# Performance work log

Measured on AMD Instinct MI355X. Metric: run time of the kernel, lower is better.

The kernel has to match this reference:

```python
import jax, jax.numpy as jnp
import numpy as np


def _butter_bandpass_ba(N, w1, w2):
    """Digital Butterworth bandpass design (scipy.signal.iirfilter equivalent),
    fs = 2 half-cycles/sample, output='ba'. Done in float64 numpy at setup time."""
    # analog lowpass prototype (buttap): no zeros, N poles on unit circle, k=1
    p = -np.exp(1j * np.pi * np.arange(-N + 1, N, 2) / (2.0 * N))
    k = 1.0
    fs = 2.0
    warped = 2.0 * fs * np.tan(np.pi * np.array([w1, w2]) / fs)
    bw = warped[1] - warped[0]
    wo = np.sqrt(warped[0] * warped[1])
    # lp2bp_zpk
    p_lp = p * bw / 2.0
    sq = np.sqrt(p_lp ** 2 - wo ** 2)
    p_bp = np.concatenate([p_lp + sq, p_lp - sq])          # 2N poles
    z_bp = np.zeros(N, dtype=complex)                       # N zeros at origin
    k_bp = k * bw ** N
    # bilinear_zpk with fs=2
    fs2 = 2.0 * fs
    z_d = (fs2 + z_bp) / (fs2 - z_bp)
    p_d = (fs2 + p_bp) / (fs2 - p_bp)
    z_d = np.concatenate([z_d, -np.ones(len(p_bp) - len(z_bp))])
    k_d = k_bp * np.real(np.prod(fs2 - z_bp) / np.prod(fs2 - p_bp))
    b = np.real(k_d * np.poly(z_d))
    a = np.real(np.poly(p_d))
    return b, a


def setup_inputs() -> dict:
    key = jax.random.key(0)
    B, T = 512, 65536
    x = jax.random.normal(key, (B, T), dtype=jnp.float32)
    b_np, a_np = _butter_bandpass_ba(4, 0.1, 0.4)           # len 9 each
    return {
        "x": x,
        "b": jnp.asarray(b_np, dtype=jnp.float32),
        "a": jnp.asarray(a_np, dtype=jnp.float32),
    }


def _lfilter(x, b, a):
    """Direct-form II transposed IIR filter with zero initial state.
    x: (B, T); b, a: (M,). Equivalent to torchaudio lfilter (clamp=False)."""
    b = b / a[0]
    a = a / a[0]
    b0 = b[0]
    bt = b[1:]          # (M-1,)
    at = a[1:]          # (M-1,)

    def step(z, xt):
        # z: (B, M-1) delay state, xt: (B,)
        y = b0 * xt + z[:, 0]
        z_new = xt[:, None] * bt[None, :] - y[:, None] * at[None, :]
        z_new = z_new.at[:, :-1].add(z[:, 1:])
        return z_new, y

    z0 = jnp.zeros((x.shape[0], b.shape[0] - 1), dtype=x.dtype)
    _, y = jax.lax.scan(step, z0, x.T)                      # y: (T, B)
    return y.T


def reference(x, b, a):
    # filtfilt: forward pass, then filter the time-reversed result and reverse back
    y = _lfilter(x, b, a)
    y = _lfilter(y[:, ::-1], b, a)[:, ::-1]
    return y
```

## Files before the change

kernel.cpp:

```cpp
#include <hip/hip_runtime.h>

constexpr int CHUNK   = 32;
constexpr int WARM    = 96;
constexpr int BLOCK   = 256;
constexpr int TILE    = BLOCK * CHUNK;
constexpr int WARM_Q  = WARM / 4;
constexpr int TILE_Q  = TILE / 4;
constexpr int STAGE_Q = TILE_Q + WARM_Q;
constexpr int QPT     = CHUNK / 4;

__device__ __forceinline__ int sw(int g) { return g ^ ((g >> 3) & 7); }

template <int DIR>
__global__ __launch_bounds__(BLOCK, 4) void iir_pass(
    const float* __restrict__ x, float* __restrict__ y,
    const float* __restrict__ bc, const float* __restrict__ ac,
    int T, int tilesPerRow)
{
    __shared__ float4 lds[STAGE_Q];

    const int tid     = threadIdx.x;
    const int row     = blockIdx.x / tilesPerRow;
    const int tileIdx = blockIdx.x - row * tilesPerRow;
    const int tileStart = tileIdx * TILE;

    const float* __restrict__ xr = x + (size_t)row * T;
    float* __restrict__       yr = y + (size_t)row * T;

    auto ld4 = [&](int s) -> float4 {
        if (s < 0) return float4{0.f, 0.f, 0.f, 0.f};
        if (DIR == 0) return *(const float4*)(xr + s);
        float4 v = *(const float4*)(xr + (T - 4 - s));
        return float4{v.w, v.z, v.y, v.x};
    };

#pragma unroll
    for (int k = 0; k < (STAGE_Q + BLOCK - 1) / BLOCK; ++k) {
        const int g = k * BLOCK + tid;
        if (g < STAGE_Q) lds[sw(g)] = ld4(tileStart - WARM + 4 * g);
    }

    const float inv = 1.0f / ac[0];
    const float b0  = bc[0] * inv;
    float bt[8], nat[8];
#pragma unroll
    for (int i = 0; i < 8; ++i) {
        bt[i]  = bc[i + 1] * inv;
        nat[i] = -(ac[i + 1] * inv);
    }

    float z[8];
#pragma unroll
    for (int i = 0; i < 8; ++i) z[i] = 0.0f;

    auto step = [&](float xv) -> float {
        const float yv = fmaf(b0, xv, z[0]);
#pragma unroll
        for (int i = 0; i < 7; ++i)
            z[i] = fmaf(nat[i], yv, fmaf(bt[i], xv, z[i + 1]));
        z[7] = fmaf(nat[7], yv, bt[7] * xv);
        return yv;
    };

    __syncthreads();

    const int gw = tid * QPT;
#pragma unroll
    for (int i = 0; i < WARM_Q; ++i) {
        const float4 q = lds[sw(gw + i)];
        step(q.x); step(q.y); step(q.z); step(q.w);
    }

    float4 out[QPT];
#pragma unroll
    for (int j = 0; j < QPT; ++j) {
        const float4 q = lds[sw(gw + WARM_Q + j)];
        float4 o;
        o.x = step(q.x); o.y = step(q.y); o.z = step(q.z); o.w = step(q.w);
        out[j] = o;
    }

    __syncthreads();

#pragma unroll
    for (int j = 0; j < QPT; ++j) lds[sw(gw + j)] = out[j];

    __syncthreads();

#pragma unroll
    for (int k = 0; k < TILE_Q / BLOCK; ++k) {
        const int q = k * BLOCK + tid;
        const float4 v = lds[sw(q)];
        const int s = tileStart + 4 * q;
        if (DIR == 0) {
            *(float4*)(yr + s) = v;
        } else {
            *(float4*)(yr + (T - 4 - s)) = float4{v.w, v.z, v.y, v.x};
        }
    }
}

extern "C" void kernel_launch(void* const* d_in, const int* in_sizes, int n_in,
                              void* d_out, int out_size, void* d_ws, size_t ws_size,
                              hipStream_t stream)
{
    const float* x = (const float*)d_in[0];
    const float* b = (const float*)d_in[1];
    const float* a = (const float*)d_in[2];
    float* out = (float*)d_out;
    float* tmp = (float*)d_ws;

    const int T = 65536;
    const int B = in_sizes[0] / T;
    const int tilesPerRow = T / TILE;
    const int totalBlocks = B * tilesPerRow;

    dim3 block(BLOCK);
    dim3 grid(totalBlocks);

    iir_pass<0><<<grid, block, 0, stream>>>(x,   tmp, b, a, T, tilesPerRow);
    iir_pass<1><<<grid, block, 0, stream>>>(tmp, out, b, a, T, tilesPerRow);
}
```

Before: 307.7 us.

## Process two chunks per thread with packed float2 FMAs and in-place LDS output

Each thread now filters two independent chunks at once using two-wide vector FMAs, aimed at the packed FP32 FMA instruction, with the block size halved so each block still covers the same tile. Output is written back in place into the LDS staging buffer rather than held in registers and rewritten after a barrier, and the store loop reads at the warm-up offset. This is meant to double instruction throughput for the serial recurrence. In exchange it doubles per-thread register state and halves the thread count per block. The extra barrier after warm-up relies on each thread's in-place writes not overlapping any other thread's reads.

```diff
diff --git a/kernel.cpp b/kernel.cpp
--- a/kernel.cpp
+++ b/kernel.cpp
@@ -2,17 +2,32 @@
 
 constexpr int CHUNK   = 32;
 constexpr int WARM    = 96;
-constexpr int BLOCK   = 256;
-constexpr int TILE    = BLOCK * CHUNK;
+constexpr int BLOCK   = 128;
+constexpr int NCHUNK  = 2 * BLOCK;
+constexpr int TILE    = NCHUNK * CHUNK;
 constexpr int WARM_Q  = WARM / 4;
 constexpr int TILE_Q  = TILE / 4;
 constexpr int STAGE_Q = TILE_Q + WARM_Q;
 constexpr int QPT     = CHUNK / 4;
 
+typedef float v2 __attribute__((ext_vector_type(2)));
+
 __device__ __forceinline__ int sw(int g) { return g ^ ((g >> 3) & 7); }
 
+__device__ __forceinline__ v2 fma2(v2 a, v2 b, v2 c) {
+#if defined(__has_builtin)
+#if __has_builtin(__builtin_elementwise_fma)
+    return __builtin_elementwise_fma(a, b, c);
+#else
+    return v2{fmaf(a.x, b.x, c.x), fmaf(a.y, b.y, c.y)};
+#endif
+#else
+    return v2{fmaf(a.x, b.x, c.x), fmaf(a.y, b.y, c.y)};
+#endif
+}
+
 template <int DIR>
-__global__ __launch_bounds__(BLOCK, 4) void iir_pass(
+__global__ __launch_bounds__(BLOCK, 2) void iir_pass(
     const float* __restrict__ x, float* __restrict__ y,
     const float* __restrict__ bc, const float* __restrict__ ac,
     int T, int tilesPerRow)
@@ -41,56 +56,64 @@
     }
 
     const float inv = 1.0f / ac[0];
-    const float b0  = bc[0] * inv;
-    float bt[8], nat[8];
+    const v2 b02 = {bc[0] * inv, bc[0] * inv};
+    v2 bt2[8], nat2[8];
 #pragma unroll
     for (int i = 0; i < 8; ++i) {
-        bt[i]  = bc[i + 1] * inv;
-        nat[i] = -(ac[i + 1] * inv);
+        const float bi = bc[i + 1] * inv;
+        const float ai = -(ac[i + 1] * inv);
+        bt2[i]  = v2{bi, bi};
+        nat2[i] = v2{ai, ai};
     }
 
-    float z[8];
+    v2 z2[8];
 #pragma unroll
-    for (int i = 0; i < 8; ++i) z[i] = 0.0f;
+    for (int i = 0; i < 8; ++i) z2[i] = v2{0.f, 0.f};
 
-    auto step = [&](float xv) -> float {
-        const float yv = fmaf(b0, xv, z[0]);
+    auto step2 = [&](v2 xv) -> v2 {
+        const v2 yv = fma2(b02, xv, z2[0]);
 #pragma unroll
         for (int i = 0; i < 7; ++i)
-            z[i] = fmaf(nat[i], yv, fmaf(bt[i], xv, z[i + 1]));
-        z[7] = fmaf(nat[7], yv, bt[7] * xv);
+            z2[i] = fma2(nat2[i], yv, fma2(bt2[i], xv, z2[i + 1]));
+        z2[7] = fma2(nat2[7], yv, bt2[7] * xv);
         return yv;
     };
 
     __syncthreads();
 
-    const int gw = tid * QPT;
+    const int gA = 8 * tid;
+    const int gB = 8 * tid + (TILE_Q / 2);
+
 #pragma unroll
     for (int i = 0; i < WARM_Q; ++i) {
-        const float4 q = lds[sw(gw + i)];
-        step(q.x); step(q.y); step(q.z); step(q.w);
-    }
-
-    float4 out[QPT];
-#pragma unroll
-    for (int j = 0; j < QPT; ++j) {
-        const float4 q = lds[sw(gw + WARM_Q + j)];
-        float4 o;
-        o.x = step(q.x); o.y = step(q.y); o.z = step(q.z); o.w = step(q.w);
-        out[j] = o;
+        const float4 qA = lds[sw(gA + i)];
+        const float4 qB = lds[sw(gB + i)];
+        step2(v2{qA.x, qB.x}); step2(v2{qA.y, qB.y});
+        step2(v2{qA.z, qB.z}); step2(v2{qA.w, qB.w});
     }
 
     __syncthreads();
 
 #pragma unroll
-    for (int j = 0; j < QPT; ++j) lds[sw(gw + j)] = out[j];
+    for (int j = 0; j < QPT; ++j) {
+        const int ia = sw(gA + WARM_Q + j);
+        const int ib = sw(gB + WARM_Q + j);
+        const float4 qA = lds[ia];
+        const float4 qB = lds[ib];
+        const v2 o0 = step2(v2{qA.x, qB.x});
+        const v2 o1 = step2(v2{qA.y, qB.y});
+        const v2 o2 = step2(v2{qA.z, qB.z});
+        const v2 o3 = step2(v2{qA.w, qB.w});
+        lds[ia] = float4{o0.x, o1.x, o2.x, o3.x};
+        lds[ib] = float4{o0.y, o1.y, o2.y, o3.y};
+    }
 
     __syncthreads();
 
 #pragma unroll
     for (int k = 0; k < TILE_Q / BLOCK; ++k) {
         const int q = k * BLOCK + tid;
-        const float4 v = lds[sw(q)];
+        const float4 v = lds[sw(q + WARM_Q)];
         const int s = tileStart + 4 * q;
         if (DIR == 0) {
             *(float4*)(yr + s) = v;
```

Measured after the change: 340.5 us. 10.7% more time.

## Make IIR blocks persistent over several tiles with double-buffered register-staged prefetch

Applied to the files above, without the earlier changes.

Each block now processes eight consecutive tiles in a loop. While it computes the current tile out of one LDS buffer, it prefetches the next tile into registers and then writes it into the second buffer. Block size drops from 256 to 128 and launch bounds from 4 to 2. The reversal for the backward pass moves from the load into the step order, and results are written back over the tile region rather than at the buffer start. The goal is to hide global load latency behind the recurrence and to cut launch and tail overhead, at the cost of fewer concurrent waves and more register and LDS pressure.

```diff
diff --git a/kernel.cpp b/kernel.cpp
--- a/kernel.cpp
+++ b/kernel.cpp
@@ -2,43 +2,26 @@
 
 constexpr int CHUNK   = 32;
 constexpr int WARM    = 96;
-constexpr int BLOCK   = 256;
+constexpr int BLOCK   = 128;
 constexpr int TILE    = BLOCK * CHUNK;
 constexpr int WARM_Q  = WARM / 4;
 constexpr int TILE_Q  = TILE / 4;
 constexpr int STAGE_Q = TILE_Q + WARM_Q;
 constexpr int QPT     = CHUNK / 4;
+constexpr int SITER   = (STAGE_Q + BLOCK - 1) / BLOCK;
 
 __device__ __forceinline__ int sw(int g) { return g ^ ((g >> 3) & 7); }
 
 template <int DIR>
-__global__ __launch_bounds__(BLOCK, 4) void iir_pass(
+__global__ __launch_bounds__(BLOCK, 2) void iir_pass(
     const float* __restrict__ x, float* __restrict__ y,
     const float* __restrict__ bc, const float* __restrict__ ac,
-    int T, int tilesPerRow)
+    int T, int tilesPerRow, int nIter)
 {
-    __shared__ float4 lds[STAGE_Q];
+    __shared__ float4 lds[2][STAGE_Q];
 
-    const int tid     = threadIdx.x;
-    const int row     = blockIdx.x / tilesPerRow;
-    const int tileIdx = blockIdx.x - row * tilesPerRow;
-    const int tileStart = tileIdx * TILE;
-
-    const float* __restrict__ xr = x + (size_t)row * T;
-    float* __restrict__       yr = y + (size_t)row * T;
-
-    auto ld4 = [&](int s) -> float4 {
-        if (s < 0) return float4{0.f, 0.f, 0.f, 0.f};
-        if (DIR == 0) return *(const float4*)(xr + s);
-        float4 v = *(const float4*)(xr + (T - 4 - s));
-        return float4{v.w, v.z, v.y, v.x};
-    };
-
-#pragma unroll
-    for (int k = 0; k < (STAGE_Q + BLOCK - 1) / BLOCK; ++k) {
-        const int g = k * BLOCK + tid;
-        if (g < STAGE_Q) lds[sw(g)] = ld4(tileStart - WARM + 4 * g);
-    }
+    const int tid       = threadIdx.x;
+    const int tileBegin = blockIdx.x * nIter;
 
     const float inv = 1.0f / ac[0];
     const float b0  = bc[0] * inv;
@@ -50,9 +33,6 @@
     }
 
     float z[8];
-#pragma unroll
-    for (int i = 0; i < 8; ++i) z[i] = 0.0f;
-
     auto step = [&](float xv) -> float {
         const float yv = fmaf(b0, xv, z[0]);
 #pragma unroll
@@ -62,41 +42,90 @@
         return yv;
     };
 
+    auto ldq = [&](const float* __restrict__ xr, int P) -> float4 {
+        if (P < 0) return float4{0.f, 0.f, 0.f, 0.f};
+        if (DIR == 0) return *(const float4*)(xr + 4 * P);
+        return *(const float4*)(xr + (T - 4 - 4 * P));
+    };
+
+    float4 vr[SITER];
+
+    auto stage_load = [&](int tg) {
+        const int row = tg / tilesPerRow;
+        const int tq0 = (tg - row * tilesPerRow) * TILE_Q;
+        const float* __restrict__ xr = x + (size_t)row * T;
+#pragma unroll
+        for (int it = 0; it < SITER; ++it) {
+            const int s = it * BLOCK + tid;
+            if (s < STAGE_Q) vr[it] = ldq(xr, tq0 + s - WARM_Q);
+        }
+    };
+    auto stage_write = [&](int buf) {
+#pragma unroll
+        for (int it = 0; it < SITER; ++it) {
+            const int s = it * BLOCK + tid;
+            if (s < STAGE_Q) lds[buf][sw(s)] = vr[it];
+        }
+    };
+
+    stage_load(tileBegin);
+    stage_write(0);
     __syncthreads();
 
-    const int gw = tid * QPT;
-#pragma unroll
-    for (int i = 0; i < WARM_Q; ++i) {
-        const float4 q = lds[sw(gw + i)];
-        step(q.x); step(q.y); step(q.z); step(q.w);
-    }
+    int cur = 0;
+    for (int k = 0; k < nIter; ++k) {
+        const int tg = tileBegin + k;
 
-    float4 out[QPT];
-#pragma unroll
-    for (int j = 0; j < QPT; ++j) {
-        const float4 q = lds[sw(gw + WARM_Q + j)];
-        float4 o;
-        o.x = step(q.x); o.y = step(q.y); o.z = step(q.z); o.w = step(q.w);
-        out[j] = o;
-    }
-
-    __syncthreads();
+        if (k + 1 < nIter) stage_load(tg + 1);
 
 #pragma unroll
-    for (int j = 0; j < QPT; ++j) lds[sw(gw + j)] = out[j];
+        for (int i = 0; i < 8; ++i) z[i] = 0.0f;
+        const int sBase = QPT * tid;
+#pragma unroll
+        for (int i = 0; i < WARM_Q; ++i) {
+            const float4 q = lds[cur][sw(sBase + i)];
+            if (DIR == 0) { step(q.x); step(q.y); step(q.z); step(q.w); }
+            else          { step(q.w); step(q.z); step(q.y); step(q.x); }
+        }
 
-    __syncthreads();
+        float4 out[QPT];
+#pragma unroll
+        for (int j = 0; j < QPT; ++j) {
+            const float4 q = lds[cur][sw(sBase + WARM_Q + j)];
+            float4 o;
+            if (DIR == 0) {
+                o.x = step(q.x); o.y = step(q.y); o.z = step(q.z); o.w = step(q.w);
+            } else {
+                o.x = step(q.w); o.y = step(q.z); o.z = step(q.y); o.w = step(q.x);
+            }
+            out[j] = o;
+        }
+
+        __syncthreads();
 
 #pragma unroll
-    for (int k = 0; k < TILE_Q / BLOCK; ++k) {
-        const int q = k * BLOCK + tid;
-        const float4 v = lds[sw(q)];
-        const int s = tileStart + 4 * q;
-        if (DIR == 0) {
-            *(float4*)(yr + s) = v;
-        } else {
-            *(float4*)(yr + (T - 4 - s)) = float4{v.w, v.z, v.y, v.x};
+        for (int j = 0; j < QPT; ++j) lds[cur][sw(sBase + WARM_Q + j)] = out[j];
+
+        __syncthreads();
+
+        {
+            const int row = tg / tilesPerRow;
+            const int tq0 = (tg - row * tilesPerRow) * TILE_Q;
+            float* __restrict__ yr = y + (size_t)row * T;
+#pragma unroll
+            for (int kk = 0; kk < TILE_Q / BLOCK; ++kk) {
+                const int s = WARM_Q + kk * BLOCK + tid;
+                const float4 q = lds[cur][sw(s)];
+                const int P = tq0 + (s - WARM_Q);
+                if (DIR == 0) *(float4*)(yr + 4 * P) = q;
+                else *(float4*)(yr + (T - 4 - 4 * P)) = float4{q.w, q.z, q.y, q.x};
+            }
         }
+
+        if (k + 1 < nIter) stage_write(cur ^ 1);
+
+        __syncthreads();
+        cur ^= 1;
     }
 }
 
@@ -113,11 +142,13 @@
     const int T = 65536;
     const int B = in_sizes[0] / T;
     const int tilesPerRow = T / TILE;
-    const int totalBlocks = B * tilesPerRow;
+    const int totalTiles  = B * tilesPerRow;
+
+    int nIter = 8;
+    if (totalTiles % nIter != 0) nIter = 1;
+    const int grid = totalTiles / nIter;
 
     dim3 block(BLOCK);
-    dim3 grid(totalBlocks);
-
-    iir_pass<0><<<grid, block, 0, stream>>>(x,   tmp, b, a, T, tilesPerRow);
-    iir_pass<1><<<grid, block, 0, stream>>>(tmp, out, b, a, T, tilesPerRow);
+    iir_pass<0><<<grid, block, 0, stream>>>(x,   tmp, b, a, T, tilesPerRow, nIter);
+    iir_pass<1><<<grid, block, 0, stream>>>(tmp, out, b, a, T, tilesPerRow, nIter);
 }
```

After: 311.8 us. Within noise of the previous version (+1.3%).
